# Optimization experiments

Hardware: AMD Instinct MI355X
Metric: run time of the kernel (lower is better)

The kernel has to match this reference:

```python
import jax, jax.numpy as jnp
import numpy as np
from jax import lax


def setup_inputs() -> dict:
    key = jax.random.key(0)
    k1, k2 = jax.random.split(key)
    X = jax.random.normal(k1, (32, 64, 112, 112), dtype=jnp.float32)
    # module draws K ~ N(0, 0.01) each forward; we materialize it as a param
    K = 0.01 * jax.random.normal(k2, (128, 64, 3, 3), dtype=jnp.float32)
    return {"X": X, "K": K}


def reference(X, K):
    # Valid-padding cross-correlation, NCHW input, OIHW kernel, no bias.
    # Matches conv2d_multi_out: sum over in_channels, stack over out_channels.
    return lax.conv_general_dilated(
        X, K,
        window_strides=(1, 1),
        padding="VALID",
        dimension_numbers=("NCHW", "OIHW", "NCHW"),
    )
```

## Files before the change

kernel.cpp:

```cpp
#include <hip/hip_runtime.h>


typedef __attribute__((ext_vector_type(8)))  _Float16 f16x8;
typedef __attribute__((ext_vector_type(16))) float    f32x16;

struct __attribute__((aligned(4))) f2u { float x, y; };

constexpr int C_IN = 64, H = 112, W = 112;
constexpr int COUT = 128, OH = 110, OW = 110;
constexpr int NIMG = 32;
constexpr int KTOT = C_IN * 9;
constexpr int OSP  = OH * OW;
constexpr int SPTOT = NIMG * OSP;
constexpr int IMG_STRIDE = C_IN * H * W;
constexpr int CH_STRIDE  = H * W;
constexpr int LDC = 72;

__device__ __forceinline__ uint pkrtz_u32(float lo, float hi) {
    union { __fp16 __attribute__((ext_vector_type(2))) h; uint u; } c;
    c.h = __builtin_amdgcn_cvt_pkrtz(lo, hi);
    return c.u;
}

__device__ __forceinline__ int swz(int row, int chw) {
    return row * LDC + (chw ^ (((row >> 1) & 7) << 3));
}

__global__ void prep_a(const float* __restrict__ Kw, _Float16* __restrict__ A16) {
    int idx = blockIdx.x * 256 + threadIdx.x;
    if (idx >= COUT * KTOT) return;
    int cout = idx / KTOT, k = idx - cout * KTOT;
    int c = k / 9, s = k - c * 9;
    int o = c >> 3, j = c & 7;
    A16[((size_t)(s * 8 + o) * COUT + cout) * 8 + j] = (_Float16)Kw[idx];
}

__global__ __launch_bounds__(512, 4)
void conv_v7(const float* __restrict__ X,
             const _Float16* __restrict__ A16,
             float* __restrict__ Out)
{
    __shared__ __align__(16) _Float16 Bs[2][128 * LDC];

    const int t = threadIdx.x;

    const int nwg = gridDim.x;
    const int q8 = nwg >> 3, r8 = nwg & 7;
    const int xcd = blockIdx.x & 7, idx8 = blockIdx.x >> 3;
    const int bid = (xcd < r8 ? xcd * (q8 + 1) : r8 * (q8 + 1) + (xcd - r8) * q8) + idx8;
    const int spBase = bid * 128;

    const int spp = t & 63;
    const int c0  = (t >> 6) << 3;
    const int sp0 = spBase + 2 * spp;
    const int nimg = sp0 / OSP;
    const int rsp  = sp0 - nimg * OSP;
    const int oh   = rsp / OW;
    const int ow   = rsp - oh * OW;
    const float* Xr = X + ((size_t)nimg * IMG_STRIDE + (size_t)c0 * CH_STRIDE + oh * W + ow);
    const int whw0 = swz(2 * spp,     c0);
    const int whw1 = swz(2 * spp + 1, c0);

    const int lane  = t & 63;
    const int wv    = t >> 6;
    const int wq    = wv >> 1;
    const int wc    = wv & 1;
    const int frow  = lane & 31;
    const int khalf = lane >> 5;
    const size_t arow = (size_t)(wq * 32 + frow) * 8;
    const int bmask = ((frow >> 1) & 7) << 3;
    const int brw0  = (wc * 64 + frow) * LDC;
    const int brw1  = (wc * 64 + 32 + frow) * LDC;

    f32x16 acc[2];
#pragma unroll
    for (int j = 0; j < 2; j++)
#pragma unroll
        for (int e = 0; e < 16; e++) acc[j][e] = 0.f;

    f2u g[8];
    f16x8 aA[4], aB[4];

#define SOFF(S) (((S) / 3) * W + ((S) % 3))

#define GATHER(S)                                                              \
    {                                                                          \
        _Pragma("unroll")                                                      \
        for (int j = 0; j < 8; j++)                                            \
            g[j] = *reinterpret_cast<const f2u*>(Xr + (size_t)j * CH_STRIDE + SOFF(S)); \
    }

#define CVTWRITE(BUF)                                                          \
    {                                                                          \
        union { uint u[4]; f16x8 v; } px, py;                                  \
        _Pragma("unroll")                                                      \
        for (int p = 0; p < 4; p++) {                                          \
            px.u[p] = pkrtz_u32(g[2 * p].x, g[2 * p + 1].x);                   \
            py.u[p] = pkrtz_u32(g[2 * p].y, g[2 * p + 1].y);                   \
        }                                                                      \
        *reinterpret_cast<f16x8*>(&Bs[BUF][whw0]) = px.v;                      \
        *reinterpret_cast<f16x8*>(&Bs[BUF][whw1]) = py.v;                      \
    }

#define ALOAD(DST, S)                                                          \
    {                                                                          \
        _Pragma("unroll")                                                      \
        for (int kk = 0; kk < 4; kk++)                                         \
            DST[kk] = *reinterpret_cast<const f16x8*>(                         \
                &A16[(size_t)(((S) * 8 + kk * 2 + khalf) * COUT) * 8 + arow]); \
    }

#define MFMA_STEP(B, AREG)                                                     \
    {                                                                          \
        _Pragma("unroll")                                                      \
        for (int kk = 0; kk < 4; kk++) {                                       \
            const int chw = (kk * 16 + khalf * 8) ^ bmask;                     \
            f16x8 b0 = *reinterpret_cast<const f16x8*>(&Bs[B][brw0 + chw]);    \
            f16x8 b1 = *reinterpret_cast<const f16x8*>(&Bs[B][brw1 + chw]);    \
            acc[0] = __builtin_amdgcn_mfma_f32_32x32x16_f16(AREG[kk], b0, acc[0], 0, 0, 0); \
            acc[1] = __builtin_amdgcn_mfma_f32_32x32x16_f16(AREG[kk], b1, acc[1], 0, 0, 0); \
        }                                                                      \
    }

#define STEP(S, CUR, NXT)                                                      \
    {                                                                          \
        ALOAD(NXT, (S) + 1);                                                   \
        CVTWRITE(((S) + 1) & 1);                                               \
        if ((S) < 7) GATHER((S) + 2);                                          \
        MFMA_STEP((S) & 1, CUR);                                               \
        __syncthreads();                                                       \
    }

    ALOAD(aA, 0);
    GATHER(0);
    CVTWRITE(0);
    GATHER(1);
    __syncthreads();

    STEP(0, aA, aB);
    STEP(1, aB, aA);
    STEP(2, aA, aB);
    STEP(3, aB, aA);
    STEP(4, aA, aB);
    STEP(5, aB, aA);
    STEP(6, aA, aB);
    STEP(7, aB, aA);
    MFMA_STEP(0, aA);

#undef GATHER
#undef CVTWRITE
#undef ALOAD
#undef MFMA_STEP
#undef STEP
#undef SOFF

#pragma unroll
    for (int j = 0; j < 2; j++) {
        const int sp2 = spBase + wc * 64 + j * 32 + frow;
        const int n2  = sp2 / OSP;
        const int r2  = sp2 - n2 * OSP;
        float* Ob = Out + (size_t)n2 * (COUT * (size_t)OSP) + r2;
        const int cbase = wq * 32 + 4 * khalf;
#pragma unroll
        for (int reg = 0; reg < 16; reg++) {
            const int crow = cbase + (reg & 3) + 8 * (reg >> 2);
            Ob[(size_t)crow * OSP] = acc[j][reg];
        }
    }
}

extern "C" void kernel_launch(void* const* d_in, const int* in_sizes, int n_in,
                              void* d_out, int out_size, void* d_ws, size_t ws_size,
                              hipStream_t stream) {
    const float* X  = (const float*)d_in[0];
    const float* Kw = (const float*)d_in[1];
    float* Out = (float*)d_out;
    _Float16* A16 = (_Float16*)d_ws;

    prep_a<<<(COUT * KTOT + 255) / 256, 256, 0, stream>>>(Kw, A16);
    conv_v7<<<SPTOT / 128, 512, 0, stream>>>(X, A16, Out);
}
```

Measured before the change: 109.9 us.

## Gather one 4-wide input row per filter row and build three shifted tiles

Each thread now loads four consecutive floats per channel per filter row and writes three column-shifted fp16 tiles into three LDS buffers. This replaces nine separate 2-float gathers with three 4-float gathers, cutting global load instructions and exploiting the horizontal overlap of the 3x3 window. The pipeline drops from 9 barrier-separated steps to 3 row phases with extra barriers, and LDS use grows by half, which may lower occupancy. Loads may also be misaligned, since ow is even but row offsets are not 16-byte aligned.

Result: slower. 123.2 us (+12.1%).

```diff
diff --git a/kernel.cpp b/kernel.cpp
--- a/kernel.cpp
+++ b/kernel.cpp
@@ -4,7 +4,7 @@
 typedef __attribute__((ext_vector_type(8)))  _Float16 f16x8;
 typedef __attribute__((ext_vector_type(16))) float    f32x16;
 
-struct __attribute__((aligned(4))) f2u { float x, y; };
+struct __attribute__((aligned(8))) f4u { float v[4]; };
 
 constexpr int C_IN = 64, H = 112, W = 112;
 constexpr int COUT = 128, OH = 110, OW = 110;
@@ -36,11 +36,11 @@
 }
 
 __global__ __launch_bounds__(512, 4)
-void conv_v7(const float* __restrict__ X,
-             const _Float16* __restrict__ A16,
-             float* __restrict__ Out)
+void conv_v11(const float* __restrict__ X,
+              const _Float16* __restrict__ A16,
+              float* __restrict__ Out)
 {
-    __shared__ __align__(16) _Float16 Bs[2][128 * LDC];
+    __shared__ __align__(16) _Float16 Bs[3][128 * LDC];
 
     const int t = threadIdx.x;
 
@@ -78,28 +78,29 @@
 #pragma unroll
         for (int e = 0; e < 16; e++) acc[j][e] = 0.f;
 
-    f2u g[8];
+    f4u G[8];
     f16x8 aA[4], aB[4];
 
-#define SOFF(S) (((S) / 3) * W + ((S) % 3))
-
-#define GATHER(S)                                                              \
+#define GATHER4(R)                                                             \
     {                                                                          \
         _Pragma("unroll")                                                      \
         for (int j = 0; j < 8; j++)                                            \
-            g[j] = *reinterpret_cast<const f2u*>(Xr + (size_t)j * CH_STRIDE + SOFF(S)); \
+            G[j] = *reinterpret_cast<const f4u*>(Xr + (size_t)j * CH_STRIDE + (R) * W); \
     }
 
-#define CVTWRITE(BUF)                                                          \
+#define CVTROW()                                                               \
     {                                                                          \
-        union { uint u[4]; f16x8 v; } px, py;                                  \
         _Pragma("unroll")                                                      \
-        for (int p = 0; p < 4; p++) {                                          \
-            px.u[p] = pkrtz_u32(g[2 * p].x, g[2 * p + 1].x);                   \
-            py.u[p] = pkrtz_u32(g[2 * p].y, g[2 * p + 1].y);                   \
+        for (int sh = 0; sh < 3; sh++) {                                       \
+            union { uint u[4]; f16x8 v; } px, py;                              \
+            _Pragma("unroll")                                                  \
+            for (int p = 0; p < 4; p++) {                                      \
+                px.u[p] = pkrtz_u32(G[2 * p].v[sh],     G[2 * p + 1].v[sh]);   \
+                py.u[p] = pkrtz_u32(G[2 * p].v[sh + 1], G[2 * p + 1].v[sh + 1]); \
+            }                                                                  \
+            *reinterpret_cast<f16x8*>(&Bs[sh][whw0]) = px.v;                   \
+            *reinterpret_cast<f16x8*>(&Bs[sh][whw1]) = py.v;                   \
         }                                                                      \
-        *reinterpret_cast<f16x8*>(&Bs[BUF][whw0]) = px.v;                      \
-        *reinterpret_cast<f16x8*>(&Bs[BUF][whw1]) = py.v;                      \
     }
 
 #define ALOAD(DST, S)                                                          \
@@ -110,49 +111,55 @@
                 &A16[(size_t)(((S) * 8 + kk * 2 + khalf) * COUT) * 8 + arow]); \
     }
 
-#define MFMA_STEP(B, AREG)                                                     \
+#define MFMA_SH(SH, AREG)                                                      \
     {                                                                          \
         _Pragma("unroll")                                                      \
         for (int kk = 0; kk < 4; kk++) {                                       \
             const int chw = (kk * 16 + khalf * 8) ^ bmask;                     \
-            f16x8 b0 = *reinterpret_cast<const f16x8*>(&Bs[B][brw0 + chw]);    \
-            f16x8 b1 = *reinterpret_cast<const f16x8*>(&Bs[B][brw1 + chw]);    \
+            f16x8 b0 = *reinterpret_cast<const f16x8*>(&Bs[SH][brw0 + chw]);   \
+            f16x8 b1 = *reinterpret_cast<const f16x8*>(&Bs[SH][brw1 + chw]);   \
             acc[0] = __builtin_amdgcn_mfma_f32_32x32x16_f16(AREG[kk], b0, acc[0], 0, 0, 0); \
             acc[1] = __builtin_amdgcn_mfma_f32_32x32x16_f16(AREG[kk], b1, acc[1], 0, 0, 0); \
         }                                                                      \
     }
 
-#define STEP(S, CUR, NXT)                                                      \
-    {                                                                          \
-        ALOAD(NXT, (S) + 1);                                                   \
-        CVTWRITE(((S) + 1) & 1);                                               \
-        if ((S) < 7) GATHER((S) + 2);                                          \
-        MFMA_STEP((S) & 1, CUR);                                               \
-        __syncthreads();                                                       \
-    }
+    GATHER4(0);
+    ALOAD(aA, 0);
 
-    ALOAD(aA, 0);
-    GATHER(0);
-    CVTWRITE(0);
-    GATHER(1);
+    CVTROW();
+    __syncthreads();
+    GATHER4(1);
+    ALOAD(aB, 1);
+    MFMA_SH(0, aA);
+    ALOAD(aA, 2);
+    MFMA_SH(1, aB);
+    ALOAD(aB, 3);
+    MFMA_SH(2, aA);
     __syncthreads();
 
-    STEP(0, aA, aB);
-    STEP(1, aB, aA);
-    STEP(2, aA, aB);
-    STEP(3, aB, aA);
-    STEP(4, aA, aB);
-    STEP(5, aB, aA);
-    STEP(6, aA, aB);
-    STEP(7, aB, aA);
-    MFMA_STEP(0, aA);
+    CVTROW();
+    __syncthreads();
+    GATHER4(2);
+    ALOAD(aA, 4);
+    MFMA_SH(0, aB);
+    ALOAD(aB, 5);
+    MFMA_SH(1, aA);
+    ALOAD(aA, 6);
+    MFMA_SH(2, aB);
+    __syncthreads();
 
-#undef GATHER
-#undef CVTWRITE
+    CVTROW();
+    __syncthreads();
+    ALOAD(aB, 7);
+    MFMA_SH(0, aA);
+    ALOAD(aA, 8);
+    MFMA_SH(1, aB);
+    MFMA_SH(2, aA);
+
+#undef GATHER4
+#undef CVTROW
 #undef ALOAD
-#undef MFMA_STEP
-#undef STEP
-#undef SOFF
+#undef MFMA_SH
 
 #pragma unroll
     for (int j = 0; j < 2; j++) {
@@ -178,5 +185,5 @@
     _Float16* A16 = (_Float16*)d_ws;
 
     prep_a<<<(COUT * KTOT + 255) / 256, 256, 0, stream>>>(Kw, A16);
-    conv_v7<<<SPTOT / 128, 512, 0, stream>>>(X, A16, Out);
+    conv_v11<<<SPTOT / 128, 512, 0, stream>>>(X, A16, Out);
 }
```

## Pre-transpose input to NHWC fp16 and stage tiles via direct global-to-LDS loads

Applied to the files above, without the earlier changes.

Adds a prep kernel that converts X to fp16 and transposes it to an NHWC layout (64 channels contiguous per pixel). The conv kernel then fills its shared-memory B tiles with global_load_lds 16-byte copies, replacing the strided fp32 gathers, register conversion and LDS stores. Bank conflicts are avoided with an XOR slot swizzle in place of the padded LDC stride. The cost is an extra pass that reads X and writes a half-size copy, plus a reworked load schedule (gather distance drops from two steps ahead to one).

Result: slower. 122.5 us (+11.5%).

```diff
diff --git a/kernel.cpp b/kernel.cpp
--- a/kernel.cpp
+++ b/kernel.cpp
@@ -4,7 +4,8 @@
 typedef __attribute__((ext_vector_type(8)))  _Float16 f16x8;
 typedef __attribute__((ext_vector_type(16))) float    f32x16;
 
-struct __attribute__((aligned(4))) f2u { float x, y; };
+typedef __attribute__((address_space(3))) uint       lds_u32;
+typedef __attribute__((address_space(1))) const uint glb_u32;
 
 constexpr int C_IN = 64, H = 112, W = 112;
 constexpr int COUT = 128, OH = 110, OW = 110;
@@ -14,16 +15,12 @@
 constexpr int SPTOT = NIMG * OSP;
 constexpr int IMG_STRIDE = C_IN * H * W;
 constexpr int CH_STRIDE  = H * W;
-constexpr int LDC = 72;
+constexpr size_t A16_BYTES = (size_t)KTOT * COUT * 2;
 
 __device__ __forceinline__ uint pkrtz_u32(float lo, float hi) {
     union { __fp16 __attribute__((ext_vector_type(2))) h; uint u; } c;
     c.h = __builtin_amdgcn_cvt_pkrtz(lo, hi);
     return c.u;
-}
-
-__device__ __forceinline__ int swz(int row, int chw) {
-    return row * LDC + (chw ^ (((row >> 1) & 7) << 3));
 }
 
 __global__ void prep_a(const float* __restrict__ Kw, _Float16* __restrict__ A16) {
@@ -35,12 +32,42 @@
     A16[((size_t)(s * 8 + o) * COUT + cout) * 8 + j] = (_Float16)Kw[idx];
 }
 
+__global__ __launch_bounds__(256, 4)
+void prep_x(const float* __restrict__ X, _Float16* __restrict__ X16t) {
+    __shared__ _Float16 L[W * 72];
+    const int t = threadIdx.x;
+    const int n = blockIdx.x / H, h = blockIdx.x - n * H;
+    const float* src = X + (size_t)n * IMG_STRIDE + (size_t)h * W;
+    const int c = t >> 2, q = t & 3;
+    const float* sc = src + (size_t)c * CH_STRIDE + q * 28;
+#pragma unroll
+    for (int v = 0; v < 7; v++) {
+        float4 f = *reinterpret_cast<const float4*>(sc + v * 4);
+        const int w0 = q * 28 + v * 4;
+        L[(w0 + 0) * 72 + c] = (_Float16)f.x;
+        L[(w0 + 1) * 72 + c] = (_Float16)f.y;
+        L[(w0 + 2) * 72 + c] = (_Float16)f.z;
+        L[(w0 + 3) * 72 + c] = (_Float16)f.w;
+    }
+    __syncthreads();
+    _Float16* dst = X16t + ((size_t)n * H + h) * W * 64;
+#pragma unroll
+    for (int r = 0; r < 4; r++) {
+        const int u = r * 256 + t;
+        if (u < 896) {
+            const int w = u >> 3, sl = u & 7;
+            *reinterpret_cast<f16x8*>(dst + (size_t)u * 8) =
+                *reinterpret_cast<const f16x8*>(&L[w * 72 + sl * 8]);
+        }
+    }
+}
+
 __global__ __launch_bounds__(512, 4)
-void conv_v7(const float* __restrict__ X,
-             const _Float16* __restrict__ A16,
-             float* __restrict__ Out)
+void conv_v12(const _Float16* __restrict__ X16t,
+              const _Float16* __restrict__ A16,
+              float* __restrict__ Out)
 {
-    __shared__ __align__(16) _Float16 Bs[2][128 * LDC];
+    __shared__ __align__(16) _Float16 Bs[2][128 * 64];
 
     const int t = threadIdx.x;
 
@@ -50,27 +77,39 @@
     const int bid = (xcd < r8 ? xcd * (q8 + 1) : r8 * (q8 + 1) + (xcd - r8) * q8) + idx8;
     const int spBase = bid * 128;
 
-    const int spp = t & 63;
-    const int c0  = (t >> 6) << 3;
-    const int sp0 = spBase + 2 * spp;
-    const int nimg = sp0 / OSP;
-    const int rsp  = sp0 - nimg * OSP;
-    const int oh   = rsp / OW;
-    const int ow   = rsp - oh * OW;
-    const float* Xr = X + ((size_t)nimg * IMG_STRIDE + (size_t)c0 * CH_STRIDE + oh * W + ow);
-    const int whw0 = swz(2 * spp,     c0);
-    const int whw1 = swz(2 * spp + 1, c0);
-
-    const int lane  = t & 63;
-    const int wv    = t >> 6;
+    const int lane = t & 63;
+    const int wv   = t >> 6;
+    const int u0 = wv * 128 + lane;
+    const int u1 = u0 + 64;
+    const _Float16* s0;
+    const _Float16* s1;
+    {
+        const int uu[2] = {u0, u1};
+        const _Float16* ss[2];
+#pragma unroll
+        for (int i = 0; i < 2; i++) {
+            const int u  = uu[i];
+            const int sp = u >> 3, slot = u & 7;
+            const int spg = spBase + sp;
+            const int n   = spg / OSP;
+            const int r   = spg - n * OSP;
+            const int oh  = r / OW;
+            const int ow  = r - oh * OW;
+            ss[i] = X16t + (((size_t)n * H + oh) * W + ow) * 64 + (slot ^ (sp & 7)) * 8;
+        }
+        s0 = ss[0]; s1 = ss[1];
+    }
+    const int l0 = u0 * 8;
+    const int l1 = u1 * 8;
+
     const int wq    = wv >> 1;
     const int wc    = wv & 1;
     const int frow  = lane & 31;
     const int khalf = lane >> 5;
     const size_t arow = (size_t)(wq * 32 + frow) * 8;
-    const int bmask = ((frow >> 1) & 7) << 3;
-    const int brw0  = (wc * 64 + frow) * LDC;
-    const int brw1  = (wc * 64 + 32 + frow) * LDC;
+    const int bmask = frow & 7;
+    const int brw0  = (wc * 64 + frow) * 64;
+    const int brw1  = brw0 + 32 * 64;
 
     f32x16 acc[2];
 #pragma unroll
@@ -78,28 +117,16 @@
 #pragma unroll
         for (int e = 0; e < 16; e++) acc[j][e] = 0.f;
 
-    f2u g[8];
     f16x8 aA[4], aB[4];
 
-#define SOFF(S) (((S) / 3) * W + ((S) % 3))
-
-#define GATHER(S)                                                              \
-    {                                                                          \
-        _Pragma("unroll")                                                      \
-        for (int j = 0; j < 8; j++)                                            \
-            g[j] = *reinterpret_cast<const f2u*>(Xr + (size_t)j * CH_STRIDE + SOFF(S)); \
-    }
-
-#define CVTWRITE(BUF)                                                          \
-    {                                                                          \
-        union { uint u[4]; f16x8 v; } px, py;                                  \
-        _Pragma("unroll")                                                      \
-        for (int p = 0; p < 4; p++) {                                          \
-            px.u[p] = pkrtz_u32(g[2 * p].x, g[2 * p + 1].x);                   \
-            py.u[p] = pkrtz_u32(g[2 * p].y, g[2 * p + 1].y);                   \
-        }                                                                      \
-        *reinterpret_cast<f16x8*>(&Bs[BUF][whw0]) = px.v;                      \
-        *reinterpret_cast<f16x8*>(&Bs[BUF][whw1]) = py.v;                      \
+#define SOFFC(S) ((((S) / 3) * W + ((S) % 3)) * 64)
+
+#define STAGE(S, B)                                                            \
+    {                                                                          \
+        __builtin_amdgcn_global_load_lds((const glb_u32*)(s0 + SOFFC(S)),      \
+                                         (lds_u32*)(&Bs[B][l0]), 16, 0, 0);    \
+        __builtin_amdgcn_global_load_lds((const glb_u32*)(s1 + SOFFC(S)),      \
+                                         (lds_u32*)(&Bs[B][l1]), 16, 0, 0);    \
     }
 
 #define ALOAD(DST, S)                                                          \
@@ -114,9 +141,9 @@
     {                                                                          \
         _Pragma("unroll")                                                      \
         for (int kk = 0; kk < 4; kk++) {                                       \
-            const int chw = (kk * 16 + khalf * 8) ^ bmask;                     \
-            f16x8 b0 = *reinterpret_cast<const f16x8*>(&Bs[B][brw0 + chw]);    \
-            f16x8 b1 = *reinterpret_cast<const f16x8*>(&Bs[B][brw1 + chw]);    \
+            const int slot = ((kk * 2 + khalf) ^ bmask) * 8;                   \
+            f16x8 b0 = *reinterpret_cast<const f16x8*>(&Bs[B][brw0 + slot]);   \
+            f16x8 b1 = *reinterpret_cast<const f16x8*>(&Bs[B][brw1 + slot]);   \
             acc[0] = __builtin_amdgcn_mfma_f32_32x32x16_f16(AREG[kk], b0, acc[0], 0, 0, 0); \
             acc[1] = __builtin_amdgcn_mfma_f32_32x32x16_f16(AREG[kk], b1, acc[1], 0, 0, 0); \
         }                                                                      \
@@ -125,16 +152,13 @@
 #define STEP(S, CUR, NXT)                                                      \
     {                                                                          \
         ALOAD(NXT, (S) + 1);                                                   \
-        CVTWRITE(((S) + 1) & 1);                                               \
-        if ((S) < 7) GATHER((S) + 2);                                          \
+        STAGE((S) + 1, ((S) + 1) & 1);                                         \
         MFMA_STEP((S) & 1, CUR);                                               \
         __syncthreads();                                                       \
     }
 
     ALOAD(aA, 0);
-    GATHER(0);
-    CVTWRITE(0);
-    GATHER(1);
+    STAGE(0, 0);
     __syncthreads();
 
     STEP(0, aA, aB);
@@ -147,12 +171,11 @@
     STEP(7, aB, aA);
     MFMA_STEP(0, aA);
 
-#undef GATHER
-#undef CVTWRITE
+#undef STAGE
 #undef ALOAD
 #undef MFMA_STEP
 #undef STEP
-#undef SOFF
+#undef SOFFC
 
 #pragma unroll
     for (int j = 0; j < 2; j++) {
@@ -175,8 +198,10 @@
     const float* X  = (const float*)d_in[0];
     const float* Kw = (const float*)d_in[1];
     float* Out = (float*)d_out;
-    _Float16* A16 = (_Float16*)d_ws;
+    _Float16* A16  = (_Float16*)d_ws;
+    _Float16* X16t = (_Float16*)((char*)d_ws + A16_BYTES);
 
     prep_a<<<(COUT * KTOT + 255) / 256, 256, 0, stream>>>(Kw, A16);
-    conv_v7<<<SPTOT / 128, 512, 0, stream>>>(X, A16, Out);
-}
+    prep_x<<<NIMG * H, 256, 0, stream>>>(X, X16t);
+    conv_v12<<<SPTOT / 128, 512, 0, stream>>>(X16t, A16, Out);
+}
```
